# Kernel tuning notes

Hardware: AMD Instinct MI355X
Metric: run time of the kernel (lower is better)

## Reference

```python
import jax, jax.numpy as jnp
import numpy as np

TEMP = 16.0  # sqrt(in_dim=256), module default when temperature=None
BN_EPS = 1e-5


def setup_inputs() -> dict:
    key = jax.random.key(0)
    ks = jax.random.split(key, 8)
    B, Cin, T, H, W = 8, 256, 8, 16, 16
    FF, Cout = 512, 256
    # small init scale keeps softmax logits in a sane range
    s = 0.02
    return {
        "x": jax.random.normal(ks[0], (B, Cin, T, H, W), jnp.float32),
        "Wk": jax.random.normal(ks[1], (FF, Cin), jnp.float32) * s,
        "Wq": jax.random.normal(ks[2], (FF, Cin), jnp.float32) * s,
        "Wv": jax.random.normal(ks[3], (FF, Cin), jnp.float32) * s,
        "Wout": jax.random.normal(ks[4], (Cout, FF), jnp.float32) * s,
        "bout": jax.random.normal(ks[5], (Cout,), jnp.float32) * s,
        "gamma": jnp.ones((Cout,), jnp.float32),
        "beta": jnp.zeros((Cout,), jnp.float32),
    }


def reference(x, Wk, Wq, Wv, Wout, bout, gamma, beta):
    B, Cin, T, H, W = x.shape
    N = T * H * W
    xf = x.reshape(B, Cin, N)                      # 1x1x1 conv == per-position matmul
    K = jnp.einsum('fc,bcn->bfn', Wk, xf)
    Q = jnp.einsum('fc,bcn->bfn', Wq, xf)
    V = jnp.einsum('fc,bcn->bfn', Wv, xf)
    KQ = jnp.einsum('bfi,bfj->bij', K, Q)          # [B, N, N] = K^T Q
    attn = jax.nn.softmax(KQ / TEMP, axis=2)
    # torch: sum(V[:, :, :, None] * attn[:, None], dim=3)
    #      = V[b,c,i] * sum_j attn[b,i,j]  (no need to materialize B x C x N x N)
    agg = V * jnp.sum(attn, axis=2)[:, None, :]    # [B, FF, N]
    o = jnp.einsum('of,bfn->bon', Wout, agg) + bout[None, :, None]
    o = jax.nn.relu(o).reshape(B, -1, T, H, W)
    y = x + o                                      # residual (in_dim == out_dim)
    # BatchNorm3d, training mode (fresh module): batch stats over (B, T, H, W)
    mean = jnp.mean(y, axis=(0, 2, 3, 4), keepdims=True)
    var = jnp.var(y, axis=(0, 2, 3, 4), keepdims=True)
    g = gamma[None, :, None, None, None]
    b = beta[None, :, None, None, None]
    return g * (y - mean) * jax.lax.rsqrt(var + BN_EPS) + b
```

## Files before the change

kernel.cpp:

```cpp
#include <hip/hip_runtime.h>

typedef __attribute__((ext_vector_type(8))) short short8;
typedef __attribute__((ext_vector_type(4))) float floatx4;

#define CIN  256
#define NSP  2048
#define COUT 256
#define FF   512
#define NSHARD 32
#define LPAD 66

__device__ unsigned short g_M[COUT * CIN];
__device__ float g_shard[NSHARD][2][COUT];

__device__ __forceinline__ unsigned short f2bf_rne(float f) {
  unsigned int u = __float_as_uint(f);
  u += 0x7fffu + ((u >> 16) & 1u);
  return (unsigned short)(u >> 16);
}

__device__ __forceinline__ unsigned int pack_bf16_hu(float lo, float hi) {
  unsigned int a = __float_as_uint(lo) + 0x8000u;
  unsigned int b = __float_as_uint(hi) + 0x8000u;
  return __builtin_amdgcn_perm(b, a, 0x07060302u);
}

__global__ __launch_bounds__(1024) void k1_m(
    const float* __restrict__ Wv, const float* __restrict__ Wout)
{
  __shared__ float ws[512];
  __shared__ float red[4][256];
  const int tid = threadIdx.x;
  const int r   = blockIdx.x;
  if (r == 0) {
    float* gs = &g_shard[0][0][0];
    #pragma unroll
    for (int i = 0; i < 16; ++i) gs[tid + i * 1024] = 0.f;
  }
  if (tid < 512) ws[tid] = Wout[(size_t)r * 512 + tid];
  __syncthreads();
  const int c  = tid & 255;
  const int fs = tid >> 8;
  float acc = 0.f;
  #pragma unroll 16
  for (int f0 = 0; f0 < 128; ++f0) {
    int f = fs * 128 + f0;
    acc += ws[f] * Wv[(size_t)f * 256 + c];
  }
  red[fs][c] = acc;
  __syncthreads();
  if (tid < 256) {
    float s = red[0][tid] + red[1][tid] + red[2][tid] + red[3][tid];
    g_M[(size_t)r * 256 + tid] = f2bf_rne(s);
  }
}

__global__ __launch_bounds__(512, 2) void k2_gemm(
    const float* __restrict__ x, const float* __restrict__ bout,
    float* __restrict__ out)
{
  __shared__ float lx[CIN * LPAD];
  __shared__ float ls[COUT], lq[COUT];
  const int tid  = threadIdx.x;
  const int lane = tid & 63;
  const int wave = tid >> 6;
  const int m16  = lane & 15;
  const int q    = lane >> 4;
  const int id   = blockIdx.x;
  const int b    = id & 7;
  const int n0   = (id >> 3) * 64;
  const int wocb = (wave & 3) * 64;
  const int wn   = (wave >> 2) * 32;

  if (tid < COUT) { ls[tid] = 0.f; lq[tid] = 0.f; }

  {
    const int n4 = (tid & 15) * 4;
    const int cr = tid >> 5;
    const int ch = (tid >> 4) & 1;
    const float* gp = x + (size_t)b * CIN * NSP + n0 + n4;
    #pragma unroll
    for (int i = 0; i < 8; ++i) {
      const int c = cr + 16 * (2 * i + ch);
      const float4 v = *(const float4*)(gp + (size_t)c * NSP);
      float* d = &lx[c * LPAD + n4];
      *(float2*)d       = make_float2(v.x, v.y);
      *(float2*)(d + 2) = make_float2(v.z, v.w);
    }
  }
  __syncthreads();

  floatx4 acc[4][2];
  #pragma unroll
  for (int i = 0; i < 4; ++i)
    #pragma unroll
    for (int j = 0; j < 2; ++j)
      acc[i][j] = (floatx4){0.f, 0.f, 0.f, 0.f};

  const unsigned short* Ab = g_M + (size_t)(wocb + m16) * 256 + q * 8;

  #pragma unroll
  for (int kk = 0; kk < 8; ++kk) {
    short8 av[4];
    #pragma unroll
    for (int ti = 0; ti < 4; ++ti)
      av[ti] = *(const short8*)(Ab + (size_t)ti * 16 * 256 + kk * 32);
    short8 bv[2];
    #pragma unroll
    for (int tj = 0; tj < 2; ++tj) {
      const int nl = wn + tj * 16 + m16;
      const float* lp = &lx[(kk * 32 + q * 8) * LPAD + nl];
      union { unsigned int u[4]; short8 v; } p;
      #pragma unroll
      for (int j = 0; j < 4; ++j) {
        float f0 = lp[(2 * j) * LPAD];
        float f1 = lp[(2 * j + 1) * LPAD];
        p.u[j] = pack_bf16_hu(f0, f1);
      }
      bv[tj] = p.v;
    }
    #pragma unroll
    for (int ti = 0; ti < 4; ++ti)
      #pragma unroll
      for (int tj = 0; tj < 2; ++tj)
        acc[ti][tj] = __builtin_amdgcn_mfma_f32_16x16x32_bf16(av[ti], bv[tj], acc[ti][tj], 0, 0, 0);
  }

  #pragma unroll
  for (int ti = 0; ti < 4; ++ti) {
    #pragma unroll
    for (int r = 0; r < 4; ++r) {
      const int oc = wocb + ti * 16 + q * 4 + r;
      const float bo = bout[oc];
      float s = 0.f, s2 = 0.f;
      #pragma unroll
      for (int tj = 0; tj < 2; ++tj) {
        const int nl = wn + tj * 16 + m16;
        const size_t gidx = ((size_t)(b * COUT + oc)) * NSP + n0 + nl;
        float o = fmaxf(acc[ti][tj][r] + bo, 0.f);
        float y = lx[oc * LPAD + nl] + o;
        out[gidx] = y;
        s += y;
        s2 += y * y;
      }
      #pragma unroll
      for (int d = 1; d < 16; d <<= 1) {
        s  += __shfl_xor(s, d, 64);
        s2 += __shfl_xor(s2, d, 64);
      }
      if (m16 == 0) {
        atomicAdd(&ls[oc], s);
        atomicAdd(&lq[oc], s2);
      }
    }
  }
  __syncthreads();
  if (tid < COUT) {
    const int s = id >> 3;
    atomicAdd(&g_shard[s][0][tid], ls[tid]);
    atomicAdd(&g_shard[s][1][tid], lq[tid]);
  }
}

__global__ __launch_bounds__(256) void k3_norm(
    const float* __restrict__ gamma, const float* __restrict__ beta,
    float* __restrict__ out)
{
  const int row = blockIdx.x;
  const int oc  = row & 255;
  float su = 0.f, sq = 0.f;
  #pragma unroll
  for (int i = 0; i < NSHARD; ++i) {
    su += g_shard[i][0][oc];
    sq += g_shard[i][1][oc];
  }
  const float inv_n = 1.f / 16384.f;
  const float m  = su * inv_n;
  const float v  = sq * inv_n - m * m;
  const float sc = gamma[oc] * rsqrtf(v + 1e-5f);
  const float sh = beta[oc] - m * sc;
  float* p = out + (size_t)row * 2048 + threadIdx.x * 8;
  float4 a = *(const float4*)p;
  float4 c = *(const float4*)(p + 4);
  a.x = a.x * sc + sh; a.y = a.y * sc + sh;
  a.z = a.z * sc + sh; a.w = a.w * sc + sh;
  c.x = c.x * sc + sh; c.y = c.y * sc + sh;
  c.z = c.z * sc + sh; c.w = c.w * sc + sh;
  *(float4*)p = a;
  *(float4*)(p + 4) = c;
}

extern "C" void kernel_launch(void* const* d_in, const int* in_sizes, int n_in,
                              void* d_out, int out_size, void* d_ws, size_t ws_size,
                              hipStream_t stream) {
  const float* x     = (const float*)d_in[0];
  const float* Wv    = (const float*)d_in[3];
  const float* Wout  = (const float*)d_in[4];
  const float* bout  = (const float*)d_in[5];
  const float* gamma = (const float*)d_in[6];
  const float* beta  = (const float*)d_in[7];
  float* out = (float*)d_out;

  hipLaunchKernelGGL(k1_m,    dim3(256),  dim3(1024), 0, stream, Wv, Wout);
  hipLaunchKernelGGL(k2_gemm, dim3(256),  dim3(512),  0, stream, x, bout, out);
  hipLaunchKernelGGL(k3_norm, dim3(2048), dim3(256),  0, stream,
                     gamma, beta, out);
}
```

Baseline: 112.9 us.

## Store x tile as pre-packed bf16 in swizzled LDS and batch M rows

The GEMM kernel now converts x to bf16 once while staging it into LDS, using a transposed, XOR-swizzled layout so each MFMA B operand is a single 16-byte LDS read instead of eight strided float reads plus packing. The smaller LDS footprint lets the launch bound allow four blocks per SM. The residual add now re-reads x from global memory instead of LDS. k1 computes four rows of M per block to reuse each Wv load, and k3 reorders its block-to-row mapping.

```diff
diff --git a/kernel.cpp b/kernel.cpp
--- a/kernel.cpp
+++ b/kernel.cpp
@@ -2,13 +2,14 @@
 
 typedef __attribute__((ext_vector_type(8))) short short8;
 typedef __attribute__((ext_vector_type(4))) float floatx4;
+typedef __attribute__((ext_vector_type(4))) unsigned int uint32x4;
 
 #define CIN  256
 #define NSP  2048
 #define COUT 256
 #define FF   512
 #define NSHARD 32
-#define LPAD 66
+#define PITCH 128
 
 __device__ unsigned short g_M[COUT * CIN];
 __device__ float g_shard[NSHARD][2][COUT];
@@ -28,38 +29,43 @@
 __global__ __launch_bounds__(1024) void k1_m(
     const float* __restrict__ Wv, const float* __restrict__ Wout)
 {
-  __shared__ float ws[512];
-  __shared__ float red[4][256];
+  __shared__ float ws[4 * FF];
+  __shared__ float red[4][4][256];
   const int tid = threadIdx.x;
-  const int r   = blockIdx.x;
-  if (r == 0) {
+  const int r0  = blockIdx.x * 4;
+  if (blockIdx.x == 0) {
     float* gs = &g_shard[0][0][0];
     #pragma unroll
     for (int i = 0; i < 16; ++i) gs[tid + i * 1024] = 0.f;
   }
-  if (tid < 512) ws[tid] = Wout[(size_t)r * 512 + tid];
+  ws[tid]        = Wout[(size_t)r0 * FF + tid];
+  ws[tid + 1024] = Wout[(size_t)r0 * FF + 1024 + tid];
   __syncthreads();
   const int c  = tid & 255;
   const int fs = tid >> 8;
-  float acc = 0.f;
-  #pragma unroll 16
+  float a0 = 0.f, a1 = 0.f, a2 = 0.f, a3 = 0.f;
+  #pragma unroll 8
   for (int f0 = 0; f0 < 128; ++f0) {
-    int f = fs * 128 + f0;
-    acc += ws[f] * Wv[(size_t)f * 256 + c];
-  }
-  red[fs][c] = acc;
-  __syncthreads();
-  if (tid < 256) {
-    float s = red[0][tid] + red[1][tid] + red[2][tid] + red[3][tid];
-    g_M[(size_t)r * 256 + tid] = f2bf_rne(s);
-  }
-}
-
-__global__ __launch_bounds__(512, 2) void k2_gemm(
+    const int f = fs * 128 + f0;
+    const float wv = Wv[(size_t)f * 256 + c];
+    a0 += ws[f] * wv;
+    a1 += ws[FF + f] * wv;
+    a2 += ws[2 * FF + f] * wv;
+    a3 += ws[3 * FF + f] * wv;
+  }
+  red[fs][0][c] = a0; red[fs][1][c] = a1;
+  red[fs][2][c] = a2; red[fs][3][c] = a3;
+  __syncthreads();
+  const int rr = tid >> 8, cc = tid & 255;
+  float s = red[0][rr][cc] + red[1][rr][cc] + red[2][rr][cc] + red[3][rr][cc];
+  g_M[(size_t)(r0 + rr) * 256 + cc] = f2bf_rne(s);
+}
+
+__global__ __launch_bounds__(512, 4) void k2_gemm(
     const float* __restrict__ x, const float* __restrict__ bout,
     float* __restrict__ out)
 {
-  __shared__ float lx[CIN * LPAD];
+  __shared__ __align__(16) unsigned int lxt[64 * PITCH];
   __shared__ float ls[COUT], lq[COUT];
   const int tid  = threadIdx.x;
   const int lane = tid & 63;
@@ -75,17 +81,24 @@
   if (tid < COUT) { ls[tid] = 0.f; lq[tid] = 0.f; }
 
   {
-    const int n4 = (tid & 15) * 4;
-    const int cr = tid >> 5;
-    const int ch = (tid >> 4) & 1;
-    const float* gp = x + (size_t)b * CIN * NSP + n0 + n4;
-    #pragma unroll
-    for (int i = 0; i < 8; ++i) {
-      const int c = cr + 16 * (2 * i + ch);
-      const float4 v = *(const float4*)(gp + (size_t)c * NSP);
-      float* d = &lx[c * LPAD + n4];
-      *(float2*)d       = make_float2(v.x, v.y);
-      *(float2*)(d + 2) = make_float2(v.z, v.w);
+    const int cgrp = tid >> 4;
+    const int n4   = tid & 15;
+    const int c0   = cgrp * 8;
+    const float* gp = x + (size_t)b * CIN * NSP + (size_t)c0 * NSP + n0 + n4 * 4;
+    float4 v[8];
+    #pragma unroll
+    for (int i = 0; i < 8; ++i)
+      v[i] = *(const float4*)(gp + (size_t)i * NSP);
+    const float* vf = (const float*)v;
+    #pragma unroll
+    for (int j = 0; j < 4; ++j) {
+      uint32x4 w;
+      #pragma unroll
+      for (int p = 0; p < 4; ++p)
+        w[p] = pack_bf16_hu(vf[(2 * p) * 4 + j], vf[(2 * p + 1) * 4 + j]);
+      const int n = n4 * 4 + j;
+      const int idx = (n * PITCH + cgrp * 4) ^ ((n & 7) << 2);
+      *(uint32x4*)&lxt[idx] = w;
     }
   }
   __syncthreads();
@@ -108,16 +121,9 @@
     short8 bv[2];
     #pragma unroll
     for (int tj = 0; tj < 2; ++tj) {
-      const int nl = wn + tj * 16 + m16;
-      const float* lp = &lx[(kk * 32 + q * 8) * LPAD + nl];
-      union { unsigned int u[4]; short8 v; } p;
-      #pragma unroll
-      for (int j = 0; j < 4; ++j) {
-        float f0 = lp[(2 * j) * LPAD];
-        float f1 = lp[(2 * j + 1) * LPAD];
-        p.u[j] = pack_bf16_hu(f0, f1);
-      }
-      bv[tj] = p.v;
+      const int n = wn + tj * 16 + m16;
+      const int idx = (n * PITCH + kk * 16 + q * 4) ^ ((n & 7) << 2);
+      bv[tj] = *(const short8*)&lxt[idx];
     }
     #pragma unroll
     for (int ti = 0; ti < 4; ++ti)
@@ -138,7 +144,7 @@
         const int nl = wn + tj * 16 + m16;
         const size_t gidx = ((size_t)(b * COUT + oc)) * NSP + n0 + nl;
         float o = fmaxf(acc[ti][tj][r] + bo, 0.f);
-        float y = lx[oc * LPAD + nl] + o;
+        float y = x[gidx] + o;
         out[gidx] = y;
         s += y;
         s2 += y * y;
@@ -166,8 +172,9 @@
     const float* __restrict__ gamma, const float* __restrict__ beta,
     float* __restrict__ out)
 {
-  const int row = blockIdx.x;
-  const int oc  = row & 255;
+  const int id = blockIdx.x;
+  const int b  = id & 7;
+  const int oc = id >> 3;
   float su = 0.f, sq = 0.f;
   #pragma unroll
   for (int i = 0; i < NSHARD; ++i) {
@@ -179,7 +186,7 @@
   const float v  = sq * inv_n - m * m;
   const float sc = gamma[oc] * rsqrtf(v + 1e-5f);
   const float sh = beta[oc] - m * sc;
-  float* p = out + (size_t)row * 2048 + threadIdx.x * 8;
+  float* p = out + ((size_t)(b * COUT + oc)) * NSP + threadIdx.x * 8;
   float4 a = *(const float4*)p;
   float4 c = *(const float4*)(p + 4);
   a.x = a.x * sc + sh; a.y = a.y * sc + sh;
@@ -201,7 +208,7 @@
   const float* beta  = (const float*)d_in[7];
   float* out = (float*)d_out;
 
-  hipLaunchKernelGGL(k1_m,    dim3(256),  dim3(1024), 0, stream, Wv, Wout);
+  hipLaunchKernelGGL(k1_m,    dim3(64),   dim3(1024), 0, stream, Wv, Wout);
   hipLaunchKernelGGL(k2_gemm, dim3(256),  dim3(512),  0, stream, x, bout, out);
   hipLaunchKernelGGL(k3_norm, dim3(2048), dim3(256),  0, stream,
                      gamma, beta, out);
```

Result: slower. 117.8 us (+4.3%).
